# Optimization experiments

Hardware: AMD Instinct MI355X
Metric: run time of the kernel (lower is better)

## Reference

```python
import jax, jax.numpy as jnp
import numpy as np
import math

B, N, D, H = 16, 200, 2048, 2048  # batch, seq (== max_len), feature dim, hidden/output dim


def setup_inputs() -> dict:
    key = jax.random.key(0)
    ks = jax.random.split(key, 16)
    s = 1.0 / math.sqrt(D)
    return {
        "input_query": jax.random.normal(ks[0], (B, N, D), jnp.float32),
        "input_key": jax.random.normal(ks[1], (B, N, D), jnp.float32),
        "input_value": jax.random.normal(ks[2], (B, N, D), jnp.float32),
        "loc_vector": jax.random.normal(ks[3], (B, N, D), jnp.float32),
        "Wq": jax.random.normal(ks[4], (D, H), jnp.float32) * s,
        "bq": jnp.zeros((H,), jnp.float32),
        "Wk": jax.random.normal(ks[5], (D, H), jnp.float32) * s,
        "bk": jnp.zeros((H,), jnp.float32),
        "Wv": jax.random.normal(ks[6], (D, H), jnp.float32) * s,
        "bv": jnp.zeros((H,), jnp.float32),
        "Wloc": jax.random.normal(ks[7], (D, H), jnp.float32) * s,
        "bloc": jnp.zeros((H,), jnp.float32),
        "Wlk": jax.random.normal(ks[8], (D, H), jnp.float32) * s,
        "blk": jnp.zeros((H,), jnp.float32),
        "param": jax.random.normal(ks[9], (B, N, H), jnp.float32),
    }


def reference(input_query, input_key, input_value, loc_vector,
              Wq, bq, Wk, bk, Wv, bv, Wloc, bloc, Wlk, blk, param):
    n = input_query.shape[1]
    lq = input_query @ Wq + bq                      # (b, n, h)
    lk = input_key @ Wk + bk                        # (b, m, h)
    lv = input_value @ Wv + bv                      # (b, m, o)
    loc = loc_vector[:, :n, :]
    lloc = loc @ Wloc + bloc                        # (b, n, h)
    kloc = loc @ Wlk + blk                          # (b, n, h)
    p = param[: input_query.shape[0], :n, :]        # (b, n, h)
    # Fused multi-term scores: (Q+P)K^T + (Q+Lloc)Kloc^T  == QK^T + Lloc Kloc^T + P K^T + Q Kloc^T
    scores = (jnp.einsum('bnh,bmh->bnm', lq + p, lk)
              + jnp.einsum('bnh,bmh->bnm', lq + lloc, kloc))
    attn = jax.nn.softmax(scores / math.sqrt(lq.shape[-1]), axis=-1)
    return jnp.einsum('bnm,bmo->bno', attn, lv)     # (b, n, o); dropout is identity in eval
```

## Files before the change

### kernel.cpp

```cpp
#include <hip/hip_runtime.h>
#include <hip/hip_bf16.h>
#include <math.h>

typedef float floatx4 __attribute__((ext_vector_type(4)));
typedef __bf16 bf16x8 __attribute__((ext_vector_type(8)));
typedef unsigned short ushort_t;

__device__ __forceinline__ ushort_t f2bf(float f) {
    union { float f; unsigned int i; } v; v.f = f;
    unsigned int i = v.i;
    return (ushort_t)((i + 0x7FFFu + ((i >> 16) & 1u)) >> 16);
}
__device__ __forceinline__ unsigned int pack2(float a, float b) {
    return (unsigned int)f2bf(a) | ((unsigned int)f2bf(b) << 16);
}
__device__ __forceinline__ floatx4 mfma16(bf16x8 a, bf16x8 b, floatx4 c) {
    return __builtin_amdgcn_mfma_f32_16x16x32_bf16(a, b, c, 0, 0, 0);
}
__device__ __forceinline__ void load_lds16(const ushort_t* g, ushort_t* l) {
    __builtin_amdgcn_global_load_lds(
        (const __attribute__((address_space(1))) unsigned int*)g,
        (__attribute__((address_space(3))) unsigned int*)l, 16, 0, 0);
}

__global__ __launch_bounds__(256) void k_convert(const float* __restrict__ q, const float* __restrict__ k,
                          const float* __restrict__ v, const float* __restrict__ loc,
                          ushort_t* qb, ushort_t* kb, ushort_t* vb, ushort_t* locb) {
    int z = blockIdx.y;
    const float* src = z == 0 ? q : z == 1 ? k : z == 2 ? v : loc;
    ushort_t* dst    = z == 0 ? qb : z == 1 ? kb : z == 2 ? vb : locb;
    size_t idx = (size_t)blockIdx.x * 256 + threadIdx.x;
    floatx4 f = *(const floatx4*)(src + idx * 4);
    uint2 o;
    o.x = pack2(f[0], f[1]);
    o.y = pack2(f[2], f[3]);
    *(uint2*)(dst + idx * 4) = o;
}

__global__ void k_wtrans(const float* __restrict__ w0, const float* __restrict__ w1,
                         const float* __restrict__ w2, const float* __restrict__ w3,
                         const float* __restrict__ w4,
                         ushort_t* t0, ushort_t* t1, ushort_t* t2, ushort_t* t3, ushort_t* t4) {
    __shared__ float tile[32][33];
    int z = blockIdx.z;
    const float* W = z == 0 ? w0 : z == 1 ? w1 : z == 2 ? w2 : z == 3 ? w3 : w4;
    ushort_t* T    = z == 0 ? t0 : z == 1 ? t1 : z == 2 ? t2 : z == 3 ? t3 : t4;
    int n0 = blockIdx.x * 32, k0 = blockIdx.y * 32;
    int tx = threadIdx.x & 31, ty = threadIdx.x >> 5;
#pragma unroll
    for (int i = 0; i < 4; i++) {
        int row = ty + i * 8;
        tile[row][tx] = W[(size_t)(k0 + row) * 2048 + n0 + tx];
    }
    __syncthreads();
#pragma unroll
    for (int i = 0; i < 4; i++) {
        int row = ty + i * 8;
        T[(size_t)(n0 + row) * 2048 + k0 + tx] = f2bf(tile[tx][row]);
    }
}

__global__ void k_vtrans(const ushort_t* __restrict__ lv, ushort_t* __restrict__ lvT) {
    __shared__ ushort_t tile[32][33];
    int n0 = blockIdx.x * 32;
    int t0 = blockIdx.y * 32;
    int b = blockIdx.z;
    int tx = threadIdx.x & 31, ty = threadIdx.x >> 5;
#pragma unroll
    for (int i = 0; i < 4; i++) {
        int row = ty + i * 8;
        int tk = t0 + row;
        ushort_t v = 0;
        if (tk < 200) v = lv[(size_t)(b * 200 + tk) * 2048 + n0 + tx];
        tile[row][tx] = v;
    }
    __syncthreads();
#pragma unroll
    for (int i = 0; i < 4; i++) {
        int row = ty + i * 8;
        lvT[((size_t)b * 2048 + n0 + row) * 224 + t0 + tx] = tile[tx][row];
    }
}

__global__ __launch_bounds__(256) void k_gemm(
    const ushort_t* A0, const ushort_t* A1, const ushort_t* A2, const ushort_t* A3, const ushort_t* A4,
    const ushort_t* W0, const ushort_t* W1, const ushort_t* W2, const ushort_t* W3, const ushort_t* W4,
    const float* B0, const float* B1, const float* B2, const float* B3, const float* B4,
    ushort_t* lqp, ushort_t* lvp, ushort_t* llocp, ushort_t* kcat) {
    int z = blockIdx.z;
    const ushort_t* A  = z == 0 ? A0 : z == 1 ? A1 : z == 2 ? A2 : z == 3 ? A3 : A4;
    const ushort_t* Wt = z == 0 ? W0 : z == 1 ? W1 : z == 2 ? W2 : z == 3 ? W3 : W4;
    const float* bias  = z == 0 ? B0 : z == 1 ? B1 : z == 2 ? B2 : z == 3 ? B3 : B4;

    const int K = 2048;
    int m0 = blockIdx.x * 128, n0 = blockIdx.y * 128;
    __shared__ ushort_t As[2][128 * 32];
    __shared__ ushort_t Bs[2][128 * 32];
    int tid = threadIdx.x;
    int lane = tid & 63, w = tid >> 6;
    int quad = lane >> 4, col = lane & 15;
    int wr = w >> 1, wc = w & 1;

    int srow0 = w * 32 + (lane >> 2);
    int srow1 = srow0 + 16;
    int skcol = (lane & 3) * 8;
    const ushort_t* Ag0 = A + (size_t)(m0 + srow0) * K + skcol;
    const ushort_t* Ag1 = A + (size_t)(m0 + srow1) * K + skcol;
    const ushort_t* Bg0 = Wt + (size_t)(n0 + srow0) * K + skcol;
    const ushort_t* Bg1 = Wt + (size_t)(n0 + srow1) * K + skcol;
    ushort_t* Asl0 = As[0] + w * 1024;
    ushort_t* Asl1 = As[1] + w * 1024;
    ushort_t* Bsl0 = Bs[0] + w * 1024;
    ushort_t* Bsl1 = Bs[1] + w * 1024;

    int aoff[4], boff[4];
#pragma unroll
    for (int i = 0; i < 4; i++) {
        aoff[i] = (wr * 64 + i * 16 + col) * 32 + quad * 8;
        boff[i] = (wc * 64 + i * 16 + col) * 32 + quad * 8;
    }

    floatx4 acc[4][4] = {};

    for (int k0 = 0; k0 < K; k0 += 64) {
        __syncthreads();
        load_lds16(Ag0 + k0, Asl0);
        load_lds16(Ag1 + k0, Asl0 + 512);
        load_lds16(Bg0 + k0, Bsl0);
        load_lds16(Bg1 + k0, Bsl0 + 512);
        load_lds16(Ag0 + k0 + 32, Asl1);
        load_lds16(Ag1 + k0 + 32, Asl1 + 512);
        load_lds16(Bg0 + k0 + 32, Bsl1);
        load_lds16(Bg1 + k0 + 32, Bsl1 + 512);
        __syncthreads();
#pragma unroll
        for (int h = 0; h < 2; h++) {
            bf16x8 af[4], bfr[4];
#pragma unroll
            for (int i = 0; i < 4; i++) af[i] = *(const bf16x8*)&As[h][aoff[i]];
#pragma unroll
            for (int i = 0; i < 4; i++) bfr[i] = *(const bf16x8*)&Bs[h][boff[i]];
#pragma unroll
            for (int mi = 0; mi < 4; mi++)
#pragma unroll
                for (int ni = 0; ni < 4; ni++)
                    acc[mi][ni] = mfma16(af[mi], bfr[ni], acc[mi][ni]);
        }
    }

    ushort_t* Cplain = z == 0 ? lqp : z == 2 ? lvp : llocp;
    int kcoff = (z == 4) ? 2048 : 0;
    bool to_kcat = (z == 1 || z == 4);
    float bvv[4];
#pragma unroll
    for (int ni = 0; ni < 4; ni++) bvv[ni] = bias[n0 + wc * 64 + ni * 16 + col];
#pragma unroll
    for (int mi = 0; mi < 4; mi++) {
#pragma unroll
        for (int r = 0; r < 4; r++) {
            int m = m0 + wr * 64 + mi * 16 + quad * 4 + r;
            ushort_t* crow;
            if (to_kcat) {
                int bb = m / 200, rr = m - bb * 200;
                crow = kcat + (size_t)(bb * 224 + rr) * 4096 + kcoff;
            } else {
                crow = Cplain + (size_t)m * 2048;
            }
#pragma unroll
            for (int ni = 0; ni < 4; ni++) {
                int n = n0 + wc * 64 + ni * 16 + col;
                crow[n] = f2bf(acc[mi][ni][r] + bvv[ni]);
            }
        }
    }
}

__global__ __launch_bounds__(256) void k_qprep(const ushort_t* __restrict__ lqp,
                                               const ushort_t* __restrict__ llocp,
                                               const float* __restrict__ param,
                                               ushort_t* __restrict__ qcat) {
    int m = blockIdx.x;
    int b = m / 200, r = m - b * 200;
    int c = threadIdx.x * 8;
    bf16x8 ql = *(const bf16x8*)(lqp + (size_t)m * 2048 + c);
    bf16x8 ll = *(const bf16x8*)(llocp + (size_t)m * 2048 + c);
    floatx4 p0 = *(const floatx4*)(param + (size_t)m * 2048 + c);
    floatx4 p1 = *(const floatx4*)(param + (size_t)m * 2048 + c + 4);
    bf16x8 q1, q2;
#pragma unroll
    for (int j = 0; j < 4; j++) {
        q1[j]     = (__bf16)((float)ql[j] + p0[j]);
        q1[j + 4] = (__bf16)((float)ql[j + 4] + p1[j]);
        q2[j]     = (__bf16)((float)ql[j] + (float)ll[j]);
        q2[j + 4] = (__bf16)((float)ql[j + 4] + (float)ll[j + 4]);
    }
    ushort_t* dst = qcat + ((size_t)(b * 224 + r)) * 4096 + c;
    *(bf16x8*)dst = q1;
    *(bf16x8*)(dst + 2048) = q2;
}

__global__ __launch_bounds__(256) void k_scores(const ushort_t* __restrict__ qcat,
                                                const ushort_t* __restrict__ kcat,
                                                float* __restrict__ part) {
    int qt = blockIdx.x;
    int b  = blockIdx.y;
    int kc = blockIdx.z;
    __shared__ ushort_t As[32 * 32];
    __shared__ ushort_t Bs[224 * 32];

    int tid = threadIdx.x;
    int lane = tid & 63, w = tid >> 6;
    int quad = lane >> 4, col = lane & 15;
    int srow = lane >> 2, scol = (lane & 3) * 8;

    const ushort_t* qbase = qcat + ((size_t)b * 224 + qt * 32) * 4096 + kc * 2048;
    const ushort_t* kbase = kcat + (size_t)b * 224 * 4096 + kc * 2048;

    const ushort_t* ssrc[4];
    ushort_t* sdst[4];
#pragma unroll
    for (int o = 0; o < 4; o++) {
        int id = w * 4 + o;
        if (id < 14) {
            ssrc[o] = kbase + (size_t)(id * 16 + srow) * 4096 + scol;
            sdst[o] = Bs + id * 512;
        } else {
            ssrc[o] = qbase + (size_t)((id - 14) * 16 + srow) * 4096 + scol;
            sdst[o] = As + (id - 14) * 512;
        }
    }

    floatx4 acc[2][4] = {};
    for (int k0 = 0; k0 < 2048; k0 += 32) {
        __syncthreads();
#pragma unroll
        for (int o = 0; o < 4; o++) load_lds16(ssrc[o] + k0, sdst[o]);
        __syncthreads();
        bf16x8 af[2];
#pragma unroll
        for (int mi = 0; mi < 2; mi++) af[mi] = *(const bf16x8*)&As[(mi * 16 + col) * 32 + quad * 8];
#pragma unroll
        for (int fi = 0; fi < 4; fi++) {
            int f = w + fi * 4;
            if (f < 14) {
                bf16x8 bf = *(const bf16x8*)&Bs[(f * 16 + col) * 32 + quad * 8];
#pragma unroll
                for (int mi = 0; mi < 2; mi++) acc[mi][fi] = mfma16(af[mi], bf, acc[mi][fi]);
            }
        }
    }

    float* pbase = part + ((size_t)(kc * 16 + b) * 224 + qt * 32) * 224;
#pragma unroll
    for (int fi = 0; fi < 4; fi++) {
        int f = w + fi * 4;
        if (f < 14) {
#pragma unroll
            for (int mi = 0; mi < 2; mi++)
#pragma unroll
                for (int r = 0; r < 4; r++)
                    pbase[(mi * 16 + quad * 4 + r) * 224 + f * 16 + col] = acc[mi][fi][r];
        }
    }
}

__global__ __launch_bounds__(256) void k_softmax(const float* __restrict__ part,
                                                 ushort_t* __restrict__ attn) {
    int row = blockIdx.x * 8 + (threadIdx.x >> 5);
    int b = row / 200, r = row - b * 200;
    int p = threadIdx.x & 31;
    const float* p0 = part + ((size_t)b * 224 + r) * 224;
    const float* p1 = p0 + (size_t)16 * 224 * 224;
    const float scale = 0.022097086912079608f;
    float ev[7];
    float mx = -1e30f;
#pragma unroll
    for (int j = 0; j < 7; j++) {
        int c = p * 7 + j;
        float v = (c < 200) ? (p0[c] + p1[c]) * scale : -1e30f;
        ev[j] = v;
        mx = fmaxf(mx, v);
    }
#pragma unroll
    for (int m = 1; m < 32; m <<= 1) mx = fmaxf(mx, __shfl_xor(mx, m, 32));
    float s = 0.f;
#pragma unroll
    for (int j = 0; j < 7; j++) {
        float e = __expf(ev[j] - mx);
        ev[j] = e;
        s += e;
    }
#pragma unroll
    for (int m = 1; m < 32; m <<= 1) s += __shfl_xor(s, m, 32);
    float rs = 1.0f / s;
    ushort_t* arow = attn + (size_t)row * 224;
#pragma unroll
    for (int j = 0; j < 7; j++) {
        int c = p * 7 + j;
        arow[c] = (c < 200) ? f2bf(ev[j] * rs) : (ushort_t)0;
    }
}

__global__ __launch_bounds__(256) void k_pv(const ushort_t* __restrict__ attn,
                                            const ushort_t* __restrict__ lvT,
                                            float* __restrict__ out) {
    int nt = blockIdx.x;
    int qt = blockIdx.y;
    int b = blockIdx.z;
    int tid = threadIdx.x, lane = tid & 63, w = tid >> 6;
    int quad = lane >> 4, col = lane & 15;
    int aq = qt * 16 + col; if (aq > 199) aq = 199;
    const ushort_t* arow = attn + (size_t)(b * 200 + aq) * 224;
    int nbase = nt * 128 + w * 32;
    const ushort_t* bp0 = lvT + ((size_t)b * 2048 + nbase + col) * 224;
    const ushort_t* bp1 = lvT + ((size_t)b * 2048 + nbase + 16 + col) * 224;
    floatx4 acc[2] = {};
#pragma unroll
    for (int k0 = 0; k0 < 224; k0 += 32) {
        int ko = k0 + quad * 8;
        bf16x8 av = *(const bf16x8*)(arow + ko);
        bf16x8 b0 = *(const bf16x8*)(bp0 + ko);
        bf16x8 b1 = *(const bf16x8*)(bp1 + ko);
        acc[0] = mfma16(av, b0, acc[0]);
        acc[1] = mfma16(av, b1, acc[1]);
    }
#pragma unroll
    for (int f = 0; f < 2; f++) {
        int n = nbase + f * 16 + col;
#pragma unroll
        for (int r = 0; r < 4; r++) {
            int m = qt * 16 + quad * 4 + r;
            if (m < 200) out[(size_t)(b * 200 + m) * 2048 + n] = acc[f][r];
        }
    }
}

extern "C" void kernel_launch(void* const* d_in, const int* in_sizes, int n_in,
                              void* d_out, int out_size, void* d_ws, size_t ws_size,
                              hipStream_t stream) {
    (void)in_sizes; (void)n_in; (void)out_size; (void)ws_size;
    const float* q    = (const float*)d_in[0];
    const float* k    = (const float*)d_in[1];
    const float* v    = (const float*)d_in[2];
    const float* loc  = (const float*)d_in[3];
    const float* Wq   = (const float*)d_in[4];
    const float* bq   = (const float*)d_in[5];
    const float* Wk   = (const float*)d_in[6];
    const float* bk   = (const float*)d_in[7];
    const float* Wv   = (const float*)d_in[8];
    const float* bv   = (const float*)d_in[9];
    const float* Wloc = (const float*)d_in[10];
    const float* bloc = (const float*)d_in[11];
    const float* Wlk  = (const float*)d_in[12];
    const float* blk  = (const float*)d_in[13];
    const float* param = (const float*)d_in[14];
    float* out = (float*)d_out;

    size_t off = 0;
    auto nxt = [&](size_t bytes) {
        void* p = (char*)d_ws + off;
        off += (bytes + 255) & ~(size_t)255;
        return p;
    };
    ushort_t* wt[5];
    for (int i = 0; i < 5; i++) wt[i] = (ushort_t*)nxt(2048ull * 2048 * 2);
    ushort_t* qb    = (ushort_t*)nxt(3200ull * 2048 * 2);
    ushort_t* kb    = (ushort_t*)nxt(3200ull * 2048 * 2);
    ushort_t* vb    = (ushort_t*)nxt(3200ull * 2048 * 2);
    ushort_t* locb  = (ushort_t*)nxt(3200ull * 2048 * 2);
    ushort_t* lqp   = (ushort_t*)nxt(3200ull * 2048 * 2);
    ushort_t* llocp = (ushort_t*)nxt(3200ull * 2048 * 2);
    ushort_t* lvp   = (ushort_t*)nxt(3200ull * 2048 * 2);
    ushort_t* kcat  = (ushort_t*)nxt(16ull * 224 * 4096 * 2);
    ushort_t* lvT  = wt[0];
    ushort_t* attn = wt[0] + 16ull * 2048 * 224;
    float*    part = (float*)((char*)d_ws + 2ull * 2048 * 2048 * 2);
    ushort_t* qcat = qb;

    k_convert<<<dim3(6400, 4), 256, 0, stream>>>(q, k, v, loc, qb, kb, vb, locb);
    k_wtrans<<<dim3(64, 64, 5), 256, 0, stream>>>(Wq, Wk, Wv, Wloc, Wlk,
                                                  wt[0], wt[1], wt[2], wt[3], wt[4]);
    k_gemm<<<dim3(25, 16, 5), 256, 0, stream>>>(qb, kb, vb, locb, locb,
                                                wt[0], wt[1], wt[2], wt[3], wt[4],
                                                bq, bk, bv, bloc, blk,
                                                lqp, lvp, llocp, kcat);
    k_qprep<<<dim3(3200), 256, 0, stream>>>(lqp, llocp, param, qcat);
    k_vtrans<<<dim3(64, 7, 16), 256, 0, stream>>>(lvp, lvT);
    k_scores<<<dim3(7, 16, 2), 256, 0, stream>>>(qcat, kcat, part);
    k_softmax<<<dim3(400), 256, 0, stream>>>(part, attn);
    k_pv<<<dim3(16, 13, 16), 256, 0, stream>>>(attn, lvT, out);
}
```

Before: 491.0 us.

## Enlarge projection GEMM tiles to 256x256 with swizzled LDS and pipelined loads

The batched projection GEMM moves from 128x128 tiles with 256 threads to 256x256 tiles with 512 threads. It adds an XOR-swizzled LDS layout to avoid bank conflicts and a software-pipelined double-buffered k-loop that uses explicit vmcnt waits, barriers and setprio around the MFMA blocks. A flattened 1D grid with an XCD-aware swizzle assigns tiles. The larger tiles give more reuse per byte loaded but leave a partial last M tile (3200 is not a multiple of 256), now guarded, and raise register pressure. The last tile reads rows past 3200, which may run past the buffer or waste work.

```diff
diff --git a/kernel.cpp b/kernel.cpp
--- a/kernel.cpp
+++ b/kernel.cpp
@@ -82,71 +82,101 @@
     }
 }
 
-__global__ __launch_bounds__(256) void k_gemm(
+#define G_SB  __builtin_amdgcn_sched_barrier(0)
+#define G_BAR __builtin_amdgcn_s_barrier()
+
+__global__ __launch_bounds__(512, 2) void k_gemm(
     const ushort_t* A0, const ushort_t* A1, const ushort_t* A2, const ushort_t* A3, const ushort_t* A4,
     const ushort_t* W0, const ushort_t* W1, const ushort_t* W2, const ushort_t* W3, const ushort_t* W4,
     const float* B0, const float* B1, const float* B2, const float* B3, const float* B4,
     ushort_t* lqp, ushort_t* lvp, ushort_t* llocp, ushort_t* kcat) {
-    int z = blockIdx.z;
+    int wg = blockIdx.x;
+    int swz = (wg & 7) * 65 + (wg >> 3);
+    int z = swz / 104;
+    int rem = swz - z * 104;
+    int ntile = rem / 13;
+    int mtile = rem - ntile * 13;
+    int m0 = mtile * 256, n0 = ntile * 256;
+
     const ushort_t* A  = z == 0 ? A0 : z == 1 ? A1 : z == 2 ? A2 : z == 3 ? A3 : A4;
     const ushort_t* Wt = z == 0 ? W0 : z == 1 ? W1 : z == 2 ? W2 : z == 3 ? W3 : W4;
     const float* bias  = z == 0 ? B0 : z == 1 ? B1 : z == 2 ? B2 : z == 3 ? B3 : B4;
 
-    const int K = 2048;
-    int m0 = blockIdx.x * 128, n0 = blockIdx.y * 128;
-    __shared__ ushort_t As[2][128 * 32];
-    __shared__ ushort_t Bs[2][128 * 32];
+    __shared__ ushort_t As[2][256 * 32];
+    __shared__ ushort_t Bs[2][256 * 32];
+
     int tid = threadIdx.x;
     int lane = tid & 63, w = tid >> 6;
     int quad = lane >> 4, col = lane & 15;
-    int wr = w >> 1, wc = w & 1;
-
-    int srow0 = w * 32 + (lane >> 2);
-    int srow1 = srow0 + 16;
-    int skcol = (lane & 3) * 8;
-    const ushort_t* Ag0 = A + (size_t)(m0 + srow0) * K + skcol;
-    const ushort_t* Ag1 = A + (size_t)(m0 + srow1) * K + skcol;
-    const ushort_t* Bg0 = Wt + (size_t)(n0 + srow0) * K + skcol;
-    const ushort_t* Bg1 = Wt + (size_t)(n0 + srow1) * K + skcol;
-    ushort_t* Asl0 = As[0] + w * 1024;
-    ushort_t* Asl1 = As[1] + w * 1024;
-    ushort_t* Bsl0 = Bs[0] + w * 1024;
-    ushort_t* Bsl1 = Bs[1] + w * 1024;
-
-    int aoff[4], boff[4];
-#pragma unroll
-    for (int i = 0; i < 4; i++) {
-        aoff[i] = (wr * 64 + i * 16 + col) * 32 + quad * 8;
-        boff[i] = (wc * 64 + i * 16 + col) * 32 + quad * 8;
-    }
-
-    floatx4 acc[4][4] = {};
-
-    for (int k0 = 0; k0 < K; k0 += 64) {
-        __syncthreads();
-        load_lds16(Ag0 + k0, Asl0);
-        load_lds16(Ag1 + k0, Asl0 + 512);
-        load_lds16(Bg0 + k0, Bsl0);
-        load_lds16(Bg1 + k0, Bsl0 + 512);
-        load_lds16(Ag0 + k0 + 32, Asl1);
-        load_lds16(Ag1 + k0 + 32, Asl1 + 512);
-        load_lds16(Bg0 + k0 + 32, Bsl1);
-        load_lds16(Bg1 + k0 + 32, Bsl1 + 512);
-        __syncthreads();
-#pragma unroll
-        for (int h = 0; h < 2; h++) {
-            bf16x8 af[4], bfr[4];
-#pragma unroll
-            for (int i = 0; i < 4; i++) af[i] = *(const bf16x8*)&As[h][aoff[i]];
-#pragma unroll
-            for (int i = 0; i < 4; i++) bfr[i] = *(const bf16x8*)&Bs[h][boff[i]];
-#pragma unroll
-            for (int mi = 0; mi < 4; mi++)
-#pragma unroll
-                for (int ni = 0; ni < 4; ni++)
-                    acc[mi][ni] = mfma16(af[mi], bfr[ni], acc[mi][ni]);
-        }
-    }
+    int wr = w >> 2, wc = w & 3;
+
+    int srow = lane >> 2;
+    int cch  = (lane & 3) ^ ((lane >> 3) & 3);
+    const ushort_t* AgB0 = A  + (size_t)(m0 + (0 * 8 + w) * 16 + srow) * 2048 + cch * 8;
+    const ushort_t* AgB1 = A  + (size_t)(m0 + (1 * 8 + w) * 16 + srow) * 2048 + cch * 8;
+    const ushort_t* BgB0 = Wt + (size_t)(n0 + (0 * 8 + w) * 16 + srow) * 2048 + cch * 8;
+    const ushort_t* BgB1 = Wt + (size_t)(n0 + (1 * 8 + w) * 16 + srow) * 2048 + cch * 8;
+    int dst0 = (0 * 8 + w) * 512;
+    int dst1 = (1 * 8 + w) * 512;
+
+#define G_STAGE(K0, B) do {                         \
+        load_lds16(AgB0 + (K0), As[B] + dst0);      \
+        load_lds16(AgB1 + (K0), As[B] + dst1);      \
+        load_lds16(BgB0 + (K0), Bs[B] + dst0);      \
+        load_lds16(BgB1 + (K0), Bs[B] + dst1);      \
+    } while (0)
+
+    int aoff[8], boff[4];
+#pragma unroll
+    for (int mi = 0; mi < 8; mi++) {
+        int row = wr * 128 + mi * 16 + col;
+        aoff[mi] = row * 32 + (quad ^ ((row >> 1) & 3)) * 8;
+    }
+#pragma unroll
+    for (int ni = 0; ni < 4; ni++) {
+        int row = wc * 64 + ni * 16 + col;
+        boff[ni] = row * 32 + (quad ^ ((row >> 1) & 3)) * 8;
+    }
+
+    floatx4 acc[8][4] = {};
+
+#define G_COMPUTE(B) do {                                                \
+        bf16x8 af[8], bfr[4];                                            \
+        _Pragma("unroll") for (int mi = 0; mi < 8; mi++)                 \
+            af[mi] = *(const bf16x8*)&As[B][aoff[mi]];                   \
+        _Pragma("unroll") for (int ni = 0; ni < 4; ni++)                 \
+            bfr[ni] = *(const bf16x8*)&Bs[B][boff[ni]];                  \
+        __builtin_amdgcn_s_setprio(1);                                   \
+        _Pragma("unroll") for (int mi = 0; mi < 8; mi++)                 \
+            _Pragma("unroll") for (int ni = 0; ni < 4; ni++)             \
+                acc[mi][ni] = mfma16(af[mi], bfr[ni], acc[mi][ni]);      \
+        __builtin_amdgcn_s_setprio(0);                                   \
+    } while (0)
+
+    G_STAGE(0, 0);
+
+#pragma unroll 1
+    for (int tt = 0; tt < 31; tt++) {
+        int k0 = tt * 64;
+        G_STAGE(k0 + 32, 1);
+        asm volatile("s_waitcnt vmcnt(4)" ::: "memory");
+        G_SB; G_BAR; G_SB;
+        G_COMPUTE(0);
+        G_SB; G_BAR;
+        G_STAGE(k0 + 64, 0);
+        asm volatile("s_waitcnt vmcnt(4)" ::: "memory");
+        G_SB; G_BAR; G_SB;
+        G_COMPUTE(1);
+        G_SB; G_BAR;
+    }
+    G_STAGE(2016, 1);
+    asm volatile("s_waitcnt vmcnt(4)" ::: "memory");
+    G_SB; G_BAR; G_SB;
+    G_COMPUTE(0);
+    G_SB; G_BAR;
+    asm volatile("s_waitcnt vmcnt(0)" ::: "memory");
+    G_SB; G_BAR; G_SB;
+    G_COMPUTE(1);
 
     ushort_t* Cplain = z == 0 ? lqp : z == 2 ? lvp : llocp;
     int kcoff = (z == 4) ? 2048 : 0;
@@ -155,24 +185,28 @@
 #pragma unroll
     for (int ni = 0; ni < 4; ni++) bvv[ni] = bias[n0 + wc * 64 + ni * 16 + col];
 #pragma unroll
-    for (int mi = 0; mi < 4; mi++) {
+    for (int mi = 0; mi < 8; mi++) {
 #pragma unroll
         for (int r = 0; r < 4; r++) {
-            int m = m0 + wr * 64 + mi * 16 + quad * 4 + r;
-            ushort_t* crow;
-            if (to_kcat) {
-                int bb = m / 200, rr = m - bb * 200;
-                crow = kcat + (size_t)(bb * 224 + rr) * 4096 + kcoff;
-            } else {
-                crow = Cplain + (size_t)m * 2048;
-            }
-#pragma unroll
-            for (int ni = 0; ni < 4; ni++) {
-                int n = n0 + wc * 64 + ni * 16 + col;
-                crow[n] = f2bf(acc[mi][ni][r] + bvv[ni]);
+            int m = m0 + wr * 128 + mi * 16 + quad * 4 + r;
+            if (m < 3200) {
+                ushort_t* crow;
+                if (to_kcat) {
+                    int bb = m / 200, rr = m - bb * 200;
+                    crow = kcat + (size_t)(bb * 224 + rr) * 4096 + kcoff;
+                } else {
+                    crow = Cplain + (size_t)m * 2048;
+                }
+#pragma unroll
+                for (int ni = 0; ni < 4; ni++) {
+                    int n = n0 + wc * 64 + ni * 16 + col;
+                    crow[n] = f2bf(acc[mi][ni][r] + bvv[ni]);
+                }
             }
         }
     }
+#undef G_STAGE
+#undef G_COMPUTE
 }
 
 __global__ __launch_bounds__(256) void k_qprep(const ushort_t* __restrict__ lqp,
@@ -380,10 +414,10 @@
     k_convert<<<dim3(6400, 4), 256, 0, stream>>>(q, k, v, loc, qb, kb, vb, locb);
     k_wtrans<<<dim3(64, 64, 5), 256, 0, stream>>>(Wq, Wk, Wv, Wloc, Wlk,
                                                   wt[0], wt[1], wt[2], wt[3], wt[4]);
-    k_gemm<<<dim3(25, 16, 5), 256, 0, stream>>>(qb, kb, vb, locb, locb,
-                                                wt[0], wt[1], wt[2], wt[3], wt[4],
-                                                bq, bk, bv, bloc, blk,
-                                                lqp, lvp, llocp, kcat);
+    k_gemm<<<dim3(520), 512, 0, stream>>>(qb, kb, vb, locb, locb,
+                                          wt[0], wt[1], wt[2], wt[3], wt[4],
+                                          bq, bk, bv, bloc, blk,
+                                          lqp, lvp, llocp, kcat);
     k_qprep<<<dim3(3200), 256, 0, stream>>>(lqp, llocp, param, qcat);
     k_vtrans<<<dim3(64, 7, 16), 256, 0, stream>>>(lvp, lvT);
     k_scores<<<dim3(7, 16, 2), 256, 0, stream>>>(qcat, kcat, part);
```

Measured after the change: 515.8 us. 1.05x slower.

## Double-buffer projection GEMM with XOR-swizzled LDS, prefetch overlap, and XCD-aware tile order

Applied to the files above, without the earlier changes.

Restructures the fused five-way projection GEMM. Each K step of 64 is staged into one LDS buffer while the other buffer is computed, using vmcnt waits and raw barriers instead of a full sync before every load. The LDS layout is XOR-swizzled to avoid bank conflicts on fragment reads, and MFMA sections run at raised wave priority. The grid is flattened to 1D with a remap that groups tiles by XCD for L2 reuse, and launch bounds request two blocks per CU. In exchange it doubles LDS use and adds an extra wraparound prefetch on the last iteration.

```diff
diff --git a/kernel.cpp b/kernel.cpp
--- a/kernel.cpp
+++ b/kernel.cpp
@@ -82,71 +82,100 @@
     }
 }
 
-__global__ __launch_bounds__(256) void k_gemm(
+#define G_SB   __builtin_amdgcn_sched_barrier(0)
+#define G_BAR  __builtin_amdgcn_s_barrier()
+#define WVM8   asm volatile("s_waitcnt vmcnt(8)" ::: "memory")
+#define WVM0   asm volatile("s_waitcnt vmcnt(0)" ::: "memory")
+
+__global__ __launch_bounds__(256, 2) void k_gemm(
     const ushort_t* A0, const ushort_t* A1, const ushort_t* A2, const ushort_t* A3, const ushort_t* A4,
     const ushort_t* W0, const ushort_t* W1, const ushort_t* W2, const ushort_t* W3, const ushort_t* W4,
     const float* B0, const float* B1, const float* B2, const float* B3, const float* B4,
     ushort_t* lqp, ushort_t* lvp, ushort_t* llocp, ushort_t* kcat) {
-    int z = blockIdx.z;
+    int bid = blockIdx.x;
+    int tileid = (bid & 7) * 250 + (bid >> 3);
+    int z = tileid / 400;
+    int r = tileid - z * 400;
+    int nt = r / 25;
+    int mt = r - nt * 25;
+    int m0 = mt * 128, n0 = nt * 128;
+
     const ushort_t* A  = z == 0 ? A0 : z == 1 ? A1 : z == 2 ? A2 : z == 3 ? A3 : A4;
     const ushort_t* Wt = z == 0 ? W0 : z == 1 ? W1 : z == 2 ? W2 : z == 3 ? W3 : W4;
     const float* bias  = z == 0 ? B0 : z == 1 ? B1 : z == 2 ? B2 : z == 3 ? B3 : B4;
 
-    const int K = 2048;
-    int m0 = blockIdx.x * 128, n0 = blockIdx.y * 128;
-    __shared__ ushort_t As[2][128 * 32];
-    __shared__ ushort_t Bs[2][128 * 32];
+    __shared__ ushort_t As[2][128 * 64];
+    __shared__ ushort_t Bs[2][128 * 64];
+
     int tid = threadIdx.x;
     int lane = tid & 63, w = tid >> 6;
     int quad = lane >> 4, col = lane & 15;
     int wr = w >> 1, wc = w & 1;
 
-    int srow0 = w * 32 + (lane >> 2);
-    int srow1 = srow0 + 16;
-    int skcol = (lane & 3) * 8;
-    const ushort_t* Ag0 = A + (size_t)(m0 + srow0) * K + skcol;
-    const ushort_t* Ag1 = A + (size_t)(m0 + srow1) * K + skcol;
-    const ushort_t* Bg0 = Wt + (size_t)(n0 + srow0) * K + skcol;
-    const ushort_t* Bg1 = Wt + (size_t)(n0 + srow1) * K + skcol;
-    ushort_t* Asl0 = As[0] + w * 1024;
-    ushort_t* Asl1 = As[1] + w * 1024;
-    ushort_t* Bsl0 = Bs[0] + w * 1024;
-    ushort_t* Bsl1 = Bs[1] + w * 1024;
-
-    int aoff[4], boff[4];
-#pragma unroll
-    for (int i = 0; i < 4; i++) {
-        aoff[i] = (wr * 64 + i * 16 + col) * 32 + quad * 8;
-        boff[i] = (wc * 64 + i * 16 + col) * 32 + quad * 8;
-    }
+    int sl = lane >> 3;
+    int sc = ((lane & 7) ^ sl) * 8;
+    const ushort_t* Ag[4]; const ushort_t* Bg[4]; int ldst[4];
+#pragma unroll
+    for (int u = 0; u < 4; u++) {
+        int rowoff = u * 32 + w * 8;
+        Ag[u] = A  + (size_t)(m0 + rowoff + sl) * 2048 + sc;
+        Bg[u] = Wt + (size_t)(n0 + rowoff + sl) * 2048 + sc;
+        ldst[u] = rowoff * 64;
+    }
+
+#define STG(KT, BUF) do { int kk = (KT) * 64;              \
+        load_lds16(Ag[0] + kk, As[BUF] + ldst[0]);         \
+        load_lds16(Ag[1] + kk, As[BUF] + ldst[1]);         \
+        load_lds16(Ag[2] + kk, As[BUF] + ldst[2]);         \
+        load_lds16(Ag[3] + kk, As[BUF] + ldst[3]);         \
+        load_lds16(Bg[0] + kk, Bs[BUF] + ldst[0]);         \
+        load_lds16(Bg[1] + kk, Bs[BUF] + ldst[1]);         \
+        load_lds16(Bg[2] + kk, Bs[BUF] + ldst[2]);         \
+        load_lds16(Bg[3] + kk, Bs[BUF] + ldst[3]); } while (0)
+
+    int sw = col & 7;
+    int ko0 = (quad ^ sw) * 8;
+    int ko1 = ((4 | quad) ^ sw) * 8;
+    int aro[4], bro[4];
+#pragma unroll
+    for (int mi = 0; mi < 4; mi++) aro[mi] = (wr * 64 + mi * 16 + col) * 64;
+#pragma unroll
+    for (int ni = 0; ni < 4; ni++) bro[ni] = (wc * 64 + ni * 16 + col) * 64;
 
     floatx4 acc[4][4] = {};
 
-    for (int k0 = 0; k0 < K; k0 += 64) {
-        __syncthreads();
-        load_lds16(Ag0 + k0, Asl0);
-        load_lds16(Ag1 + k0, Asl0 + 512);
-        load_lds16(Bg0 + k0, Bsl0);
-        load_lds16(Bg1 + k0, Bsl0 + 512);
-        load_lds16(Ag0 + k0 + 32, Asl1);
-        load_lds16(Ag1 + k0 + 32, Asl1 + 512);
-        load_lds16(Bg0 + k0 + 32, Bsl1);
-        load_lds16(Bg1 + k0 + 32, Bsl1 + 512);
-        __syncthreads();
-#pragma unroll
-        for (int h = 0; h < 2; h++) {
-            bf16x8 af[4], bfr[4];
-#pragma unroll
-            for (int i = 0; i < 4; i++) af[i] = *(const bf16x8*)&As[h][aoff[i]];
-#pragma unroll
-            for (int i = 0; i < 4; i++) bfr[i] = *(const bf16x8*)&Bs[h][boff[i]];
-#pragma unroll
-            for (int mi = 0; mi < 4; mi++)
-#pragma unroll
-                for (int ni = 0; ni < 4; ni++)
-                    acc[mi][ni] = mfma16(af[mi], bfr[ni], acc[mi][ni]);
-        }
-    }
+#define CMP(BUF) do {                                                     \
+        bf16x8 af[4][2], bfr[4][2];                                       \
+        _Pragma("unroll") for (int mi = 0; mi < 4; mi++) {                \
+            af[mi][0] = *(const bf16x8*)&As[BUF][aro[mi] + ko0];          \
+            af[mi][1] = *(const bf16x8*)&As[BUF][aro[mi] + ko1]; }        \
+        _Pragma("unroll") for (int ni = 0; ni < 4; ni++) {                \
+            bfr[ni][0] = *(const bf16x8*)&Bs[BUF][bro[ni] + ko0];         \
+            bfr[ni][1] = *(const bf16x8*)&Bs[BUF][bro[ni] + ko1]; }       \
+        __builtin_amdgcn_s_setprio(1);                                    \
+        _Pragma("unroll") for (int mi = 0; mi < 4; mi++)                  \
+        _Pragma("unroll") for (int ni = 0; ni < 4; ni++) {                \
+            acc[mi][ni] = mfma16(af[mi][0], bfr[ni][0], acc[mi][ni]);     \
+            acc[mi][ni] = mfma16(af[mi][1], bfr[ni][1], acc[mi][ni]); }   \
+        __builtin_amdgcn_s_setprio(0); } while (0)
+
+    STG(0, 0);
+
+#pragma unroll 1
+    for (int tt = 0; tt < 16; tt++) {
+        int t0k = tt * 2;
+        STG(t0k + 1, 1);
+        WVM8;
+        G_SB; G_BAR; G_SB;
+        CMP(0);
+        G_SB; G_BAR;
+        STG((t0k + 2) & 31, 0);
+        WVM8;
+        G_SB; G_BAR; G_SB;
+        CMP(1);
+        G_SB; G_BAR;
+    }
+    WVM0;
 
     ushort_t* Cplain = z == 0 ? lqp : z == 2 ? lvp : llocp;
     int kcoff = (z == 4) ? 2048 : 0;
@@ -157,8 +186,8 @@
 #pragma unroll
     for (int mi = 0; mi < 4; mi++) {
 #pragma unroll
-        for (int r = 0; r < 4; r++) {
-            int m = m0 + wr * 64 + mi * 16 + quad * 4 + r;
+        for (int r2 = 0; r2 < 4; r2++) {
+            int m = m0 + wr * 64 + mi * 16 + quad * 4 + r2;
             ushort_t* crow;
             if (to_kcat) {
                 int bb = m / 200, rr = m - bb * 200;
@@ -169,10 +198,12 @@
 #pragma unroll
             for (int ni = 0; ni < 4; ni++) {
                 int n = n0 + wc * 64 + ni * 16 + col;
-                crow[n] = f2bf(acc[mi][ni][r] + bvv[ni]);
+                crow[n] = f2bf(acc[mi][ni][r2] + bvv[ni]);
             }
         }
     }
+#undef STG
+#undef CMP
 }
 
 __global__ __launch_bounds__(256) void k_qprep(const ushort_t* __restrict__ lqp,
@@ -380,10 +411,10 @@
     k_convert<<<dim3(6400, 4), 256, 0, stream>>>(q, k, v, loc, qb, kb, vb, locb);
     k_wtrans<<<dim3(64, 64, 5), 256, 0, stream>>>(Wq, Wk, Wv, Wloc, Wlk,
                                                   wt[0], wt[1], wt[2], wt[3], wt[4]);
-    k_gemm<<<dim3(25, 16, 5), 256, 0, stream>>>(qb, kb, vb, locb, locb,
-                                                wt[0], wt[1], wt[2], wt[3], wt[4],
-                                                bq, bk, bv, bloc, blk,
-                                                lqp, lvp, llocp, kcat);
+    k_gemm<<<dim3(2000), 256, 0, stream>>>(qb, kb, vb, locb, locb,
+                                           wt[0], wt[1], wt[2], wt[3], wt[4],
+                                           bq, bk, bv, bloc, blk,
+                                           lqp, lvp, llocp, kcat);
     k_qprep<<<dim3(3200), 256, 0, stream>>>(lqp, llocp, param, qcat);
     k_vtrans<<<dim3(64, 7, 16), 256, 0, stream>>>(lvp, lvT);
     k_scores<<<dim3(7, 16, 2), 256, 0, stream>>>(qcat, kcat, part);
```

New measurement: 472.2 us. -3.8%, faster.
